# Kernel optimization log

Hardware: AMD Instinct MI355X
Metric: run time of the kernel (lower is better)

Reference implementation:

```python
import jax, jax.numpy as jnp
import numpy as np

B, INDIM, OUTDIM = 1024, 2048, 4096


def setup_inputs() -> dict:
    key = jax.random.key(0)
    kx, kw, kb = jax.random.split(key, 3)
    x = jax.random.normal(kx, (B, INDIM), dtype=jnp.float32)
    # nn.Linear(indim, outdim): weight [outdim, indim], bias [outdim]
    bound = 1.0 / np.sqrt(INDIM)
    W = jax.random.uniform(kw, (OUTDIM, INDIM), minval=-bound, maxval=bound, dtype=jnp.float32)
    b = jax.random.uniform(kb, (OUTDIM,), minval=-bound, maxval=bound, dtype=jnp.float32)
    return {"x": x, "W": W, "b": b}


def reference(x, W, b):
    # Faithful to torch: prototypes = weight.transpose(0,1).reshape(outdim, indim)
    # (a reflatten of W^T, not the original weight rows, since outdim != indim).
    protos = W.T.reshape(W.shape[0], W.shape[1])  # [outdim, indim]
    # -||x_i - p_j||^2 - b_j via GEMM identity (same math as broadcast subtract + norm^2)
    x_sq = jnp.sum(x * x, axis=1, keepdims=True)          # [B, 1]
    p_sq = jnp.sum(protos * protos, axis=1)[None, :]      # [1, outdim]
    xp = jnp.einsum('bd,od->bo', x, protos)               # [B, outdim]
    return -(x_sq - 2.0 * xp + p_sq) - b[None, :]
```

## Files before the change

### kernel.cpp

```cpp
#include <hip/hip_runtime.h>

#define IN_DIM  2048
#define OUT_DIM 4096

typedef float     f32x4 __attribute__((ext_vector_type(4)));
typedef long long llx2  __attribute__((ext_vector_type(2)));

__device__ __forceinline__ unsigned int pk4(float a, float b, float c, float d) {
    int v = __builtin_amdgcn_cvt_pk_fp8_f32(a, b, 0, false);
    v     = __builtin_amdgcn_cvt_pk_fp8_f32(c, d, v, true);
    return (unsigned int)v;
}

__device__ __forceinline__ void async16(const void* g, void* l) {
    __builtin_amdgcn_global_load_lds(
        (const __attribute__((address_space(1))) unsigned int*)g,
        (__attribute__((address_space(3))) unsigned int*)l,
        16, 0, 0);
}

__device__ __forceinline__ int gmem_of(int c) { return 2 * (c & 3) + (c >> 2); }

extern "C" __global__ __launch_bounds__(256) void prep(
        const float* __restrict__ W, const float* __restrict__ x,
        unsigned char* __restrict__ protos, unsigned char* __restrict__ xb,
        float* __restrict__ psq_part, float* __restrict__ x_sq) {
    __shared__ float tile[64][65];
    const int t = threadIdx.x;

    if (blockIdx.z == 2) {
        const int b = blockIdx.x + 32 * blockIdx.y;
        const float* xp = x + (size_t)b * IN_DIM + t * 8;
        const float4 v0 = ((const float4*)xp)[0];
        const float4 v1 = ((const float4*)xp)[1];
        uint2 pk;
        pk.x = pk4(v0.x, v0.y, v0.z, v0.w);
        pk.y = pk4(v1.x, v1.y, v1.z, v1.w);
        *(uint2*)(xb + (size_t)b * IN_DIM + (t >> 3) * 64 + gmem_of(t & 7) * 8) = pk;

        float s = v0.x * v0.x + v0.y * v0.y + v0.z * v0.z + v0.w * v0.w
                + v1.x * v1.x + v1.y * v1.y + v1.z * v1.z + v1.w * v1.w;
#pragma unroll
        for (int off = 32; off > 0; off >>= 1) s += __shfl_down(s, off);
        const int lane = t & 63, w = t >> 6;
        if (lane == 0) tile[0][w] = s;
        __syncthreads();
        if (t == 0) x_sq[b] = tile[0][0] + tile[0][1] + tile[0][2] + tile[0][3];
        return;
    }

    const int r  = blockIdx.z;
    const int c0 = blockIdx.x * 64;
    const int d0 = blockIdx.y * 64;
    const int g  = t >> 4;
    const int cc = (t & 15) * 4;

    const float* Wp = W + (size_t)(r * IN_DIM + d0 + g) * IN_DIM + c0 + cc;
#pragma unroll
    for (int p = 0; p < 4; ++p) {
        const float4 v = *(const float4*)(Wp + (size_t)(16 * p) * IN_DIM);
        const int dl = g + 16 * p;
        tile[dl][cc]     = v.x;
        tile[dl][cc + 1] = v.y;
        tile[dl][cc + 2] = v.z;
        tile[dl][cc + 3] = v.w;
    }
    __syncthreads();

    const int c8 = t & 7;
    const int gm = gmem_of(c8);
#pragma unroll
    for (int p = 0; p < 2; ++p) {
        const int cr = (t >> 3) + 32 * p;
        float v[8];
        float ss = 0.f;
#pragma unroll
        for (int j = 0; j < 8; ++j) {
            v[j] = tile[8 * c8 + j][cr];
            ss += v[j] * v[j];
        }
        const int o = 2 * (c0 + cr) + r;
        uint2 pk;
        pk.x = pk4(16.f * v[0], 16.f * v[1], 16.f * v[2], 16.f * v[3]);
        pk.y = pk4(16.f * v[4], 16.f * v[5], 16.f * v[6], 16.f * v[7]);
        *(uint2*)(protos + (size_t)o * IN_DIM + d0 + gm * 8) = pk;
        ss += __shfl_xor(ss, 1);
        ss += __shfl_xor(ss, 2);
        ss += __shfl_xor(ss, 4);
        if (c8 == 0) psq_part[(size_t)blockIdx.y * OUT_DIM + o] = ss;
    }
}

extern "C" __global__ __launch_bounds__(256, 4) void gemm_epi(
        const unsigned char* __restrict__ A,
        const unsigned char* __restrict__ Bt,
        const float* __restrict__ x_sq,
        const float* __restrict__ psq_part,
        const float* __restrict__ bias,
        float* __restrict__ out) {
    __shared__ __align__(16) unsigned char smem[16384];
    unsigned char* lA = smem;
    unsigned char* lB = smem + 8192;

    const int lid = blockIdx.x;
    const int xcd = lid & 7;
    const int wi  = lid >> 3;
    const int nt  = xcd * 8 + (wi & 7);
    const int mt  = wi >> 3;
    const int m0 = mt * 64;
    const int n0 = nt * 64;

    const int t = threadIdx.x;
    const int rS = t >> 3;
    const int pS = t & 7;
    const int lS = pS ^ (rS & 7);
    const size_t goff = (size_t)(lS >> 2) * 1024 + (lS & 3) * 16;
    const unsigned char* gA0 = A  + (size_t)(m0 + rS) * IN_DIM + goff;
    const unsigned char* gA1 = gA0 + (size_t)32 * IN_DIM;
    const unsigned char* gB0 = Bt + (size_t)(n0 + rS) * IN_DIM + goff;
    const unsigned char* gB1 = gB0 + (size_t)32 * IN_DIM;
    unsigned char* lAd = lA + t * 16;
    unsigned char* lBd = lB + t * 16;

    const int wave = t >> 6;
    const int lane = t & 63;
    const int kh = wave & 1;
    const int nh = wave >> 1;
    const int ln = lane & 15;
    const int qd = lane >> 4;
    const int pr = (kh * 4 + qd) ^ (ln & 7);

    f32x4 acc[4][2] = {};

    for (int it = 0; it < 16; ++it) {
        async16(gA0, lAd); async16(gA1, lAd + 4096);
        async16(gB0, lBd); async16(gB1, lBd + 4096);
        gA0 += 64; gA1 += 64; gB0 += 64; gB1 += 64;
        __syncthreads();

        llx2 af[4], bf[2];
#pragma unroll
        for (int i = 0; i < 4; ++i)
            af[i] = *(const llx2*)(lA + (i * 16 + ln) * 128 + pr * 16);
#pragma unroll
        for (int j = 0; j < 2; ++j)
            bf[j] = *(const llx2*)(lB + (nh * 32 + j * 16 + ln) * 128 + pr * 16);
#pragma unroll
        for (int kk = 0; kk < 2; ++kk)
#pragma unroll
            for (int i = 0; i < 4; ++i)
#pragma unroll
                for (int j = 0; j < 2; ++j)
                    acc[i][j] = __builtin_amdgcn_mfma_f32_16x16x32_fp8_fp8(
                                    af[i][kk], bf[j][kk], acc[i][j], 0, 0, 0);
        __syncthreads();
    }

    if (kh == 1) {
#pragma unroll
        for (int i = 0; i < 4; ++i)
#pragma unroll
            for (int j = 0; j < 2; ++j)
                *(f32x4*)(smem + nh * 8192 + (i * 2 + j) * 1024 + lane * 16) =
                    acc[i][j];
    }
    __syncthreads();
    if (kh == 0) {
#pragma unroll
        for (int j = 0; j < 2; ++j) {
            const int col = n0 + nh * 32 + j * 16 + ln;
            float pb = bias[col];
#pragma unroll
            for (int dt = 0; dt < 32; ++dt)
                pb += psq_part[(size_t)dt * OUT_DIM + col];
#pragma unroll
            for (int i = 0; i < 4; ++i) {
                const f32x4 o4 = *(const f32x4*)(smem + nh * 8192 +
                                                 (i * 2 + j) * 1024 + lane * 16);
                const int row0 = m0 + i * 16 + qd * 4;
#pragma unroll
                for (int rr = 0; rr < 4; ++rr) {
                    const int row = row0 + rr;
                    out[(size_t)row * OUT_DIM + col] =
                        0.125f * (acc[i][j][rr] + o4[rr]) - x_sq[row] - pb;
                }
            }
        }
    }
}

extern "C" void kernel_launch(void* const* d_in, const int* in_sizes, int n_in,
                              void* d_out, int out_size, void* d_ws, size_t ws_size,
                              hipStream_t stream) {
    const float* x    = (const float*)d_in[0];
    const float* W    = (const float*)d_in[1];
    const float* bias = (const float*)d_in[2];
    float* out = (float*)d_out;

    char* ws = (char*)d_ws;
    unsigned char* protos = (unsigned char*)ws;
    unsigned char* xb     = (unsigned char*)(ws + (size_t)8 * 1024 * 1024);
    float* x_sq           = (float*)(ws + (size_t)10 * 1024 * 1024);
    float* psq_part       = (float*)(ws + (size_t)10 * 1024 * 1024 + 65536);

    prep<<<dim3(32, 32, 3), 256, 0, stream>>>(W, x, protos, xb, psq_part, x_sq);
    gemm_epi<<<dim3(1024), 256, 0, stream>>>(xb, protos, x_sq, psq_part, bias, out);
}
```

Measured before the change: 108.1 us.

## Double-buffer LDS tiles in FP8 GEMM to overlap global loads with MFMA

The GEMM kernel's shared buffer doubles to 32 KB and alternates between two stages. The next K-slice is prefetched with async global-to-LDS loads while the current one is consumed. Manual vmcnt waits and raw barriers replace __syncthreads so the in-flight loads can cross the barrier. The larger LDS footprint may reduce occupancy, and the hand-written waitcnt logic depends on the compiler not reordering the memory operations.

```diff
diff --git a/kernel.cpp b/kernel.cpp
--- a/kernel.cpp
+++ b/kernel.cpp
@@ -98,9 +98,7 @@
         const float* __restrict__ psq_part,
         const float* __restrict__ bias,
         float* __restrict__ out) {
-    __shared__ __align__(16) unsigned char smem[16384];
-    unsigned char* lA = smem;
-    unsigned char* lB = smem + 8192;
+    __shared__ __align__(16) unsigned char smem[32768];
 
     const int lid = blockIdx.x;
     const int xcd = lid & 7;
@@ -119,8 +117,6 @@
     const unsigned char* gA1 = gA0 + (size_t)32 * IN_DIM;
     const unsigned char* gB0 = Bt + (size_t)(n0 + rS) * IN_DIM + goff;
     const unsigned char* gB1 = gB0 + (size_t)32 * IN_DIM;
-    unsigned char* lAd = lA + t * 16;
-    unsigned char* lBd = lB + t * 16;
 
     const int wave = t >> 6;
     const int lane = t & 63;
@@ -132,12 +128,30 @@
 
     f32x4 acc[4][2] = {};
 
+    async16(gA0, smem + t * 16);
+    async16(gA1, smem + 4096 + t * 16);
+    async16(gB0, smem + 8192 + t * 16);
+    async16(gB1, smem + 12288 + t * 16);
+    gA0 += 64; gA1 += 64; gB0 += 64; gB1 += 64;
+
+    int bb = 0;
     for (int it = 0; it < 16; ++it) {
-        async16(gA0, lAd); async16(gA1, lAd + 4096);
-        async16(gB0, lBd); async16(gB1, lBd + 4096);
-        gA0 += 64; gA1 += 64; gB0 += 64; gB1 += 64;
-        __syncthreads();
-
+        const int nb = bb ^ 16384;
+        if (it < 15) {
+            async16(gA0, smem + nb + t * 16);
+            async16(gA1, smem + nb + 4096 + t * 16);
+            async16(gB0, smem + nb + 8192 + t * 16);
+            async16(gB1, smem + nb + 12288 + t * 16);
+            gA0 += 64; gA1 += 64; gB0 += 64; gB1 += 64;
+            asm volatile("s_waitcnt vmcnt(4)" ::: "memory");
+        } else {
+            asm volatile("s_waitcnt vmcnt(0)" ::: "memory");
+        }
+        __builtin_amdgcn_s_barrier();
+        __builtin_amdgcn_sched_barrier(0);
+
+        const unsigned char* lA = smem + bb;
+        const unsigned char* lB = smem + bb + 8192;
         llx2 af[4], bf[2];
 #pragma unroll
         for (int i = 0; i < 4; ++i)
@@ -153,7 +167,9 @@
                 for (int j = 0; j < 2; ++j)
                     acc[i][j] = __builtin_amdgcn_mfma_f32_16x16x32_fp8_fp8(
                                     af[i][kk], bf[j][kk], acc[i][j], 0, 0, 0);
-        __syncthreads();
+        __builtin_amdgcn_s_barrier();
+        __builtin_amdgcn_sched_barrier(0);
+        bb = nb;
     }
 
     if (kh == 1) {
```

After: 116.6 us. 7.9% more time.
